# Kernel tuning notes

Hardware: AMD Instinct MI355X
Metric: run time of the kernel (lower is better)

## Reference

```python
import jax, jax.numpy as jnp
import numpy as np

DIM = 1024
H = 16
DH = DIM // H
K = 4
B = 8
N = 2048
EPS = 1e-6


def _depthwise_conv_silu(x, w, n):
    # x: (B, N, C), w: (C, 1, K)  -- torch Conv1d depthwise, padding=K//2, truncate to n, SiLU
    pad = K // 2
    y = jax.lax.conv_general_dilated(
        x.transpose(0, 2, 1), w, window_strides=(1,), padding=[(pad, pad)],
        dimension_numbers=('NCH', 'OIH', 'NCH'), feature_group_count=x.shape[-1])
    y = y[..., :n]  # for even K the conv output is n+1; torch truncates
    return jax.nn.silu(y).transpose(0, 2, 1)


def _l2norm(x):
    return x / (jnp.linalg.norm(x, axis=-1, keepdims=True) + EPS)


def setup_inputs() -> dict:
    key = jax.random.key(0)
    ks = jax.random.split(key, 16)
    s = 1.0 / np.sqrt(DIM)
    d = dict(
        x=jax.random.normal(ks[0], (B, N, DIM), jnp.float32),
        Wq=jax.random.normal(ks[1], (DIM, DIM), jnp.float32) * s,
        bq=jnp.zeros((DIM,), jnp.float32),
        Wk=jax.random.normal(ks[2], (DIM, DIM), jnp.float32) * s,
        bk=jnp.zeros((DIM,), jnp.float32),
        Wv=jax.random.normal(ks[3], (DIM, DIM), jnp.float32) * s,
        bv=jnp.zeros((DIM,), jnp.float32),
        Wa=jax.random.normal(ks[4], (H, DIM), jnp.float32) * s,
        ba=jnp.zeros((H,), jnp.float32),
        Wb=jax.random.normal(ks[5], (H, DIM), jnp.float32) * s,
        bb=jnp.zeros((H,), jnp.float32),
        conv_q=jax.random.normal(ks[6], (DIM, 1, K), jnp.float32) * 0.5,
        conv_k=jax.random.normal(ks[7], (DIM, 1, K), jnp.float32) * 0.5,
        conv_v=jax.random.normal(ks[8], (DIM, 1, K), jnp.float32) * 0.5,
        Wo=jax.random.normal(ks[9], (DIM, DIM), jnp.float32) * s,
        bo=jnp.zeros((DIM,), jnp.float32),
    )
    return d


def _forward(x, Wq, bq, Wk, bk, Wv, bv, Wa, ba, Wb, bb, conv_q, conv_k, conv_v, Wo, bo):
    b_, n_, c_ = x.shape
    q = _l2norm(_depthwise_conv_silu(jax.nn.silu(x @ Wq.T + bq), conv_q, n_))
    k = _l2norm(_depthwise_conv_silu(jax.nn.silu(x @ Wk.T + bk), conv_k, n_))
    v = _depthwise_conv_silu(jax.nn.silu(x @ Wv.T + bv), conv_v, n_)
    a = jax.nn.sigmoid(x @ Wa.T + ba)  # (B, N, H)
    bgate = jax.nn.sigmoid(x @ Wb.T + bb)  # (B, N, H)

    # (N, B, H, Dh) for scan over time
    q = q.reshape(b_, n_, H, DH).transpose(1, 0, 2, 3)
    k = k.reshape(b_, n_, H, DH).transpose(1, 0, 2, 3)
    v = v.reshape(b_, n_, H, DH).transpose(1, 0, 2, 3)
    a = a.transpose(1, 0, 2)
    bgate = bgate.transpose(1, 0, 2)

    S0 = jnp.zeros((b_, H, DH, DH), x.dtype)

    def step(S, inp):
        qt, kt, vt, at, bt = inp  # qt/kt/vt: (B,H,Dh), at/bt: (B,H)
        at = at[..., None, None]
        bt = bt[..., None, None]
        # S_new = S @ (a*(I - b k k^T)) + b * v k^T
        #       = a*S - a*b*(S k) k^T + b * v k^T
        Sk = jnp.einsum('bhde,bhe->bhd', S, kt)
        outer_Sk_k = Sk[..., :, None] * kt[..., None, :]
        outer_v_k = vt[..., :, None] * kt[..., None, :]
        S_new = at * S - at * bt * outer_Sk_k + bt * outer_v_k
        # o_e = sum_d q_d S[d, e]
        ot = jnp.einsum('bhd,bhde->bhe', qt, S_new)
        return S_new, ot

    _, O = jax.lax.scan(step, S0, (q, k, v, a, bgate))  # O: (N, B, H, Dh)
    O = O.transpose(1, 0, 2, 3).reshape(b_, n_, c_)
    return O @ Wo.T + bo


def reference(x, Wq, bq, Wk, bk, Wv, bv, Wa, ba, Wb, bb, conv_q, conv_k, conv_v, Wo, bo):
    return _forward(x, Wq, bq, Wk, bk, Wv, bv, Wa, ba, Wb, bb, conv_q, conv_k, conv_v, Wo, bo)
```

## Files before the change

kernel.cpp:

```cpp
#include <hip/hip_runtime.h>

#define DIMC 1024
#define SEQ  2048
#define NHEAD 16
#define BATCH 8

__device__ __forceinline__ void gll4(const float* g, float* l) {
  __builtin_amdgcn_global_load_lds(
      (const __attribute__((address_space(1))) void*)g,
      (__attribute__((address_space(3))) void*)l, 4, 0, 0);
}
__device__ __forceinline__ void gll16(const unsigned short* g, unsigned short* l) {
  __builtin_amdgcn_global_load_lds(
      (const __attribute__((address_space(1))) void*)g,
      (__attribute__((address_space(3))) void*)l, 16, 0, 0);
}

#define WAIT_VM45   0x8F7D
#define WAIT_VM0    0x0F70

__device__ __forceinline__ unsigned short f2bf(float f) {
  unsigned u = __float_as_uint(f);
  return (unsigned short)((u + 0x7fffu + ((u >> 16) & 1u)) >> 16);
}
__device__ __forceinline__ float bf2f(unsigned short h) {
  return __uint_as_float(((unsigned)h) << 16);
}

typedef __attribute__((ext_vector_type(8))) short  bf16x8;
typedef __attribute__((ext_vector_type(4))) float  floatx4;

__device__ __forceinline__ float oct_sum(float x) {
  int t1 = __builtin_amdgcn_update_dpp(0, __float_as_int(x), 0xB1, 0xF, 0xF, true);
  float x1 = x + __int_as_float(t1);
  int t2 = __builtin_amdgcn_update_dpp(0, __float_as_int(x1), 0x4E, 0xF, 0xF, true);
  float x2 = x1 + __int_as_float(t2);
  int t3 = __builtin_amdgcn_update_dpp(0, __float_as_int(x2), 0x141, 0xF, 0xF, true);
  return x2 + __int_as_float(t3);
}

__global__ __launch_bounds__(256)
void cvt_split(const float* __restrict__ in, unsigned short* __restrict__ hi,
               unsigned short* __restrict__ lo, int n4)
{
  int i = blockIdx.x * 256 + threadIdx.x;
  if (i >= n4) return;
  float4 f = ((const float4*)in)[i];
  unsigned short h0 = f2bf(f.x), h1 = f2bf(f.y), h2 = f2bf(f.z), h3 = f2bf(f.w);
  unsigned short l0 = f2bf(f.x - bf2f(h0)), l1 = f2bf(f.y - bf2f(h1));
  unsigned short l2 = f2bf(f.z - bf2f(h2)), l3 = f2bf(f.w - bf2f(h3));
  ushort4 H; H.x = h0; H.y = h1; H.z = h2; H.w = h3;
  ushort4 L; L.x = l0; L.y = l1; L.z = l2; L.w = l3;
  ((ushort4*)hi)[i] = H;
  ((ushort4*)lo)[i] = L;
}

__global__ void pack_ab_kernel(const float* __restrict__ Wa, const float* __restrict__ ba,
                               const float* __restrict__ Wb, const float* __restrict__ bb,
                               float* __restrict__ Wab, float* __restrict__ bab)
{
  int i = blockIdx.x * 256 + threadIdx.x;
  if (i < 128 * 1024) {
    int row = i >> 10, col = i & 1023;
    float v = 0.0f;
    if (row < 16) v = Wa[(row << 10) + col];
    else if (row < 32) v = Wb[((row - 16) << 10) + col];
    Wab[i] = v;
  } else {
    int j = i - 128 * 1024;
    if (j < 128) {
      float v = 0.0f;
      if (j < 16) v = ba[j];
      else if (j < 32) v = bb[j - 16];
      bab[j] = v;
    }
  }
}

__global__ __launch_bounds__(256, 2)
void gemm_bf16x3(const unsigned short* __restrict__ Ah, const unsigned short* __restrict__ Al,
                 const unsigned short* __restrict__ Bh, const unsigned short* __restrict__ Bl,
                 const float* __restrict__ bias, float* __restrict__ C,
                 int K, int ldc, int nvalid, int act)
{
  __shared__ unsigned short sAh[4096], sAl[4096], sBh[4096], sBl[4096];
  const int tid  = threadIdx.x;
  const int lane = tid & 63;
  const int w    = tid >> 6;

  const int crow = tid >> 2;
  const int kel  = (tid & 3) << 3;
  const unsigned short* pAh0 = Ah + (size_t)(blockIdx.x * 128 + crow) * K + kel;
  const unsigned short* pAh1 = Ah + (size_t)(blockIdx.x * 128 + 64 + crow) * K + kel;
  const unsigned short* pAl0 = Al + (size_t)(blockIdx.x * 128 + crow) * K + kel;
  const unsigned short* pAl1 = Al + (size_t)(blockIdx.x * 128 + 64 + crow) * K + kel;
  const unsigned short* pBh0 = Bh + (size_t)(blockIdx.y * 128 + crow) * K + kel;
  const unsigned short* pBh1 = Bh + (size_t)(blockIdx.y * 128 + 64 + crow) * K + kel;
  const unsigned short* pBl0 = Bl + (size_t)(blockIdx.y * 128 + crow) * K + kel;
  const unsigned short* pBl1 = Bl + (size_t)(blockIdx.y * 128 + 64 + crow) * K + kel;
  const int wb = (tid & 192) * 8;

  floatx4 acc[16];
  #pragma unroll
  for (int i = 0; i < 16; ++i) acc[i] = (floatx4){0.f, 0.f, 0.f, 0.f};

  const int mq = (w & 1) << 6;
  const int nq = (w >> 1) << 6;
  const int fr = lane & 15;
  const int fk = (lane >> 4) << 3;

  for (int kt = 0; kt < K; kt += 32) {
    __syncthreads();
    gll16(pAh0, sAh + wb); gll16(pAh1, sAh + 2048 + wb);
    gll16(pAl0, sAl + wb); gll16(pAl1, sAl + 2048 + wb);
    gll16(pBh0, sBh + wb); gll16(pBh1, sBh + 2048 + wb);
    gll16(pBl0, sBl + wb); gll16(pBl1, sBl + 2048 + wb);
    pAh0 += 32; pAh1 += 32; pAl0 += 32; pAl1 += 32;
    pBh0 += 32; pBh1 += 32; pBl0 += 32; pBl1 += 32;
    __syncthreads();

    bf16x8 ah[4], al[4], bh[4], bl[4];
    #pragma unroll
    for (int mi = 0; mi < 4; ++mi) {
      int off = (mq + mi * 16 + fr) * 32 + fk;
      ah[mi] = *(const bf16x8*)&sAh[off];
      al[mi] = *(const bf16x8*)&sAl[off];
    }
    #pragma unroll
    for (int ni = 0; ni < 4; ++ni) {
      int off = (nq + ni * 16 + fr) * 32 + fk;
      bh[ni] = *(const bf16x8*)&sBh[off];
      bl[ni] = *(const bf16x8*)&sBl[off];
    }
    #pragma unroll
    for (int mi = 0; mi < 4; ++mi)
      #pragma unroll
      for (int ni = 0; ni < 4; ++ni) {
        floatx4 c = acc[mi * 4 + ni];
        c = __builtin_amdgcn_mfma_f32_16x16x32_bf16(ah[mi], bh[ni], c, 0, 0, 0);
        c = __builtin_amdgcn_mfma_f32_16x16x32_bf16(ah[mi], bl[ni], c, 0, 0, 0);
        c = __builtin_amdgcn_mfma_f32_16x16x32_bf16(al[mi], bh[ni], c, 0, 0, 0);
        acc[mi * 4 + ni] = c;
      }
  }

  const int mbase = blockIdx.x * 128 + mq + ((lane >> 4) << 2);
  const int nbase = blockIdx.y * 128 + nq + (lane & 15);
  #pragma unroll
  for (int ni = 0; ni < 4; ++ni) {
    int n = nbase + ni * 16;
    if (n < nvalid) {
      float bs = bias[n];
      #pragma unroll
      for (int mi = 0; mi < 4; ++mi) {
        #pragma unroll
        for (int r = 0; r < 4; ++r) {
          int m = mbase + mi * 16 + r;
          float val = acc[mi * 4 + ni][r] + bs;
          if (act == 1)      val = val * (1.0f / (1.0f + __expf(-val)));
          else if (act == 2) val = 1.0f / (1.0f + __expf(-val));
          C[(size_t)m * ldc + n] = val;
        }
      }
    }
  }
}

__global__ __launch_bounds__(256)
void conv_kernel(const float* __restrict__ pre, const float* __restrict__ w,
                 float* __restrict__ out, int do_norm)
{
  __shared__ float red[4];
  const int bt  = blockIdx.x;
  const int t   = bt & (SEQ - 1);
  const int tid = threadIdx.x;
  const int c   = tid << 2;
  const float* rowp = pre + (size_t)bt * DIMC + c;
  const float4 z = make_float4(0.f, 0.f, 0.f, 0.f);
  float4 xm2 = (t >= 2)      ? *(const float4*)(rowp - 2 * DIMC) : z;
  float4 xm1 = (t >= 1)      ? *(const float4*)(rowp - DIMC)     : z;
  float4 x0  =                 *(const float4*)(rowp);
  float4 xp1 = (t + 1 < SEQ) ? *(const float4*)(rowp + DIMC)     : z;
  const float4 w0 = *(const float4*)(w + (size_t)(c + 0) * 4);
  const float4 w1 = *(const float4*)(w + (size_t)(c + 1) * 4);
  const float4 w2 = *(const float4*)(w + (size_t)(c + 2) * 4);
  const float4 w3 = *(const float4*)(w + (size_t)(c + 3) * 4);
  float y0 = xm2.x * w0.x + xm1.x * w0.y + x0.x * w0.z + xp1.x * w0.w;
  float y1 = xm2.y * w1.x + xm1.y * w1.y + x0.y * w1.z + xp1.y * w1.w;
  float y2 = xm2.z * w2.x + xm1.z * w2.y + x0.z * w2.z + xp1.z * w2.w;
  float y3 = xm2.w * w3.x + xm1.w * w3.y + x0.w * w3.z + xp1.w * w3.w;
  y0 = y0 * (1.0f / (1.0f + __expf(-y0)));
  y1 = y1 * (1.0f / (1.0f + __expf(-y1)));
  y2 = y2 * (1.0f / (1.0f + __expf(-y2)));
  y3 = y3 * (1.0f / (1.0f + __expf(-y3)));
  if (do_norm) {
    float ss = y0*y0 + y1*y1 + y2*y2 + y3*y3;
    #pragma unroll
    for (int off = 32; off >= 1; off >>= 1) ss += __shfl_xor(ss, off);
    if ((tid & 63) == 0) red[tid >> 6] = ss;
    __syncthreads();
    float tot = red[0] + red[1] + red[2] + red[3];
    float rn = 1.0f / (sqrtf(tot) + 1e-6f);
    y0 *= rn; y1 *= rn; y2 *= rn; y3 *= rn;
  }
  *(float4*)(out + (size_t)bt * DIMC + c) = make_float4(y0, y1, y2, y3);
}

#define PD 16
__global__ __launch_bounds__(64)
void scan2_kernel(const float* __restrict__ k, const float* __restrict__ v,
                  const float* __restrict__ ab, float* __restrict__ Cf,
                  float* __restrict__ SC)
{
  __shared__ float ring[PD][2][64];
  __shared__ float aS[SEQ];
  __shared__ float bSh[SEQ];
  const int blk = blockIdx.x;
  const int bh  = blk >> 3;
  const int dg  = blk & 7;
  const int b   = bh >> 4, h = bh & 15;
  const int tid = threadIdx.x;
  const int dl  = tid >> 3;
  const int eh  = tid & 7;
  const int d   = dg * 8 + dl;
  const int e0  = eh * 8;

  const float* abbase = ab + (size_t)b * SEQ * 32 + h;
  for (int i = tid; i < SEQ; i += 64) {
    aS[i]  = abbase[(size_t)i * 32];
    bSh[i] = abbase[(size_t)i * 32 + 16];
  }

  const size_t base = (size_t)b * SEQ * DIMC + h * 64;
  const float* kp = k + base + tid;
  const float* vp = v + base + tid;

  {
    float4 z4 = make_float4(0.f, 0.f, 0.f, 0.f);
    float4* dst0 = (float4*)&SC[(((size_t)bh * 32) * 64 + d) * 64 + e0];
    dst0[0] = z4; dst0[1] = z4;
  }

  #pragma unroll
  for (int pt = 0; pt < PD; ++pt) {
    gll4(kp + (size_t)pt * DIMC, &ring[pt][0][0]);
    gll4(vp + (size_t)pt * DIMC, &ring[pt][1][0]);
  }
  __builtin_amdgcn_s_waitcnt(WAIT_VM0);
  asm volatile("" ::: "memory");

  float S[8];
  #pragma unroll
  for (int j = 0; j < 8; ++j) S[j] = 0.f;

  float* cfp = Cf + (size_t)bh * SEQ * 64 + d;

  float4 ka  = *(const float4*)&ring[0][0][e0];
  float4 kb8 = *(const float4*)&ring[0][0][e0 + 4];
  float  vd  = ring[0][1][d];
  float  a   = aS[0];
  float  bg  = bSh[0];

  for (int t = 0; t < SEQ; ++t) {
    float p0 = fmaf(S[0], ka.x, S[4] * kb8.x);
    float p1 = fmaf(S[1], ka.y, S[5] * kb8.y);
    float p2 = fmaf(S[2], ka.z, S[6] * kb8.z);
    float p3 = fmaf(S[3], ka.w, S[7] * kb8.w);
    float sk = oct_sum((p0 + p1) + (p2 + p3));
    const float coef = fmaf(-a * bg, sk, bg * vd);
    if (eh == 0) cfp[(size_t)t * 64] = coef;
    asm volatile("" ::: "memory");

    if (t < SEQ - PD) {
      const int slot = t & (PD - 1);
      gll4(kp + (size_t)(t + PD) * DIMC, &ring[slot][0][0]);
      gll4(vp + (size_t)(t + PD) * DIMC, &ring[slot][1][0]);
      asm volatile("" ::: "memory");
      __builtin_amdgcn_s_waitcnt(WAIT_VM45);
    } else {
      asm volatile("" ::: "memory");
      __builtin_amdgcn_s_waitcnt(WAIT_VM0);
    }
    asm volatile("" ::: "memory");

    const int sl1 = (t + 1) & (PD - 1);
    const int tn  = (t + 1) & (SEQ - 1);
    const float4 ka_n  = *(const float4*)&ring[sl1][0][e0];
    const float4 kb_n  = *(const float4*)&ring[sl1][0][e0 + 4];
    const float  vd_n  = ring[sl1][1][d];
    const float  a_n   = aS[tn];
    const float  b_n   = bSh[tn];

    S[0] = fmaf(a, S[0], coef * ka.x);
    S[1] = fmaf(a, S[1], coef * ka.y);
    S[2] = fmaf(a, S[2], coef * ka.z);
    S[3] = fmaf(a, S[3], coef * ka.w);
    S[4] = fmaf(a, S[4], coef * kb8.x);
    S[5] = fmaf(a, S[5], coef * kb8.y);
    S[6] = fmaf(a, S[6], coef * kb8.z);
    S[7] = fmaf(a, S[7], coef * kb8.w);

    if (((t + 1) & 63) == 0 && (t + 1) < SEQ) {
      float4* dst = (float4*)&SC[(((size_t)bh * 32 + ((t + 1) >> 6)) * 64 + d) * 64 + e0];
      dst[0] = make_float4(S[0], S[1], S[2], S[3]);
      dst[1] = make_float4(S[4], S[5], S[6], S[7]);
    }

    ka = ka_n; kb8 = kb_n; vd = vd_n; a = a_n; bg = b_n;
  }
}

__global__ __launch_bounds__(256)
void outp_kernel(const float* __restrict__ q, const float* __restrict__ k,
                 const float* __restrict__ Cf, const float* __restrict__ SC,
                 const float* __restrict__ ab, float* __restrict__ O)
{
  __shared__ float QsT[64 * 64];
  __shared__ float CP [64 * 64];
  __shared__ float Ks [64 * 64];
  __shared__ float Zs [64 * 64];
  __shared__ float av[64], Gv[64], rGv[64];

  const int c   = blockIdx.x;
  const int bh  = blockIdx.y;
  const int b   = bh >> 4, h = bh & 15;
  const int cs  = c << 6;
  const int tid = threadIdx.x;
  const int tl  = tid & 63, th = tid >> 6;

  {
    const float* qr = q  + ((size_t)(b * SEQ + cs + tl)) * DIMC + h * 64 + th * 16;
    const float* cr = Cf + ((size_t)bh * SEQ + cs + tl) * 64 + th * 16;
    #pragma unroll
    for (int u = 0; u < 4; ++u) {
      float4 qv = *(const float4*)(qr + u * 4);
      float4 cv = *(const float4*)(cr + u * 4);
      int dd = th * 16 + u * 4;
      QsT[(dd+0)*64 + tl] = qv.x; QsT[(dd+1)*64 + tl] = qv.y;
      QsT[(dd+2)*64 + tl] = qv.z; QsT[(dd+3)*64 + tl] = qv.w;
      CP [(dd+0)*64 + tl] = cv.x; CP [(dd+1)*64 + tl] = cv.y;
      CP [(dd+2)*64 + tl] = cv.z; CP [(dd+3)*64 + tl] = cv.w;
    }
    const float* kr = k  + ((size_t)(b * SEQ + cs + tl)) * DIMC + h * 64 + th * 16;
    const float* zr = SC + (((size_t)bh * 32 + c) * 64 + tl) * 64 + th * 16;
    #pragma unroll
    for (int u = 0; u < 4; ++u) {
      *(float4*)&Ks[tl * 64 + th * 16 + u * 4] = *(const float4*)(kr + u * 4);
      *(float4*)&Zs[tl * 64 + th * 16 + u * 4] = *(const float4*)(zr + u * 4);
    }
    if (tid < 64) av[tid] = ab[((size_t)(b * SEQ + cs + tid)) * 32 + h];
  }
  __syncthreads();
  if (tid == 0) {
    float g = 1.f;
    for (int t = 0; t < 64; ++t) { g *= av[t]; Gv[t] = fmaxf(g, 1e-37f); }
  }
  __syncthreads();
  if (tid < 64) rGv[tid] = 1.0f / Gv[tid];
  __syncthreads();

  const int tq = (tid >> 4) << 2;
  const int s0 = (tid & 15) << 2;

  float p[4][4] = {{0.f}};
  #pragma unroll 4
  for (int dd = 0; dd < 64; ++dd) {
    const float4 qv = *(const float4*)&QsT[dd * 64 + tq];
    const float4 cv = *(const float4*)&CP [dd * 64 + s0];
    const float qa[4] = {qv.x, qv.y, qv.z, qv.w};
    const float ca[4] = {cv.x, cv.y, cv.z, cv.w};
    #pragma unroll
    for (int i = 0; i < 4; ++i)
      #pragma unroll
      for (int j = 0; j < 4; ++j)
        p[i][j] = fmaf(qa[i], ca[j], p[i][j]);
  }
  __syncthreads();

  #pragma unroll
  for (int i = 0; i < 4; ++i) {
    const float gt = Gv[tq + i];
    #pragma unroll
    for (int j = 0; j < 4; ++j) {
      float vsc = (s0 + j <= tq + i) ? p[i][j] * gt * rGv[s0 + j] : 0.f;
      CP[(s0 + j) * 64 + (tq + i)] = vsc;
    }
  }
  __syncthreads();

  const int e0 = s0;
  float o[4][4] = {{0.f}};
  #pragma unroll 4
  for (int ss = 0; ss < 64; ++ss) {
    const float4 pv = *(const float4*)&CP[ss * 64 + tq];
    const float4 kv = *(const float4*)&Ks[ss * 64 + e0];
    const float pa[4] = {pv.x, pv.y, pv.z, pv.w};
    const float ka[4] = {kv.x, kv.y, kv.z, kv.w};
    #pragma unroll
    for (int i = 0; i < 4; ++i)
      #pragma unroll
      for (int j = 0; j < 4; ++j)
        o[i][j] = fmaf(pa[i], ka[j], o[i][j]);
  }
  float zt[4][4] = {{0.f}};
  #pragma unroll 4
  for (int dd = 0; dd < 64; ++dd) {
    const float4 qv = *(const float4*)&QsT[dd * 64 + tq];
    const float4 zv = *(const float4*)&Zs[dd * 64 + e0];
    const float qa[4] = {qv.x, qv.y, qv.z, qv.w};
    const float za[4] = {zv.x, zv.y, zv.z, zv.w};
    #pragma unroll
    for (int i = 0; i < 4; ++i)
      #pragma unroll
      for (int j = 0; j < 4; ++j)
        zt[i][j] = fmaf(qa[i], za[j], zt[i][j]);
  }
  #pragma unroll
  for (int i = 0; i < 4; ++i) {
    const float gt = Gv[tq + i];
    float4 res;
    res.x = fmaf(gt, zt[i][0], o[i][0]);
    res.y = fmaf(gt, zt[i][1], o[i][1]);
    res.z = fmaf(gt, zt[i][2], o[i][2]);
    res.w = fmaf(gt, zt[i][3], o[i][3]);
    *(float4*)(O + ((size_t)(b * SEQ + cs + tq + i)) * DIMC + h * 64 + e0) = res;
  }
}

extern "C" void kernel_launch(void* const* d_in, const int* in_sizes, int n_in,
                              void* d_out, int out_size, void* d_ws, size_t ws_size,
                              hipStream_t stream)
{
  const float* x  = (const float*)d_in[0];
  const float* Wq = (const float*)d_in[1];
  const float* bq = (const float*)d_in[2];
  const float* Wk = (const float*)d_in[3];
  const float* bk = (const float*)d_in[4];
  const float* Wv = (const float*)d_in[5];
  const float* bv = (const float*)d_in[6];
  const float* Wa = (const float*)d_in[7];
  const float* ba = (const float*)d_in[8];
  const float* Wb = (const float*)d_in[9];
  const float* bb = (const float*)d_in[10];
  const float* cq = (const float*)d_in[11];
  const float* ck = (const float*)d_in[12];
  const float* cv = (const float*)d_in[13];
  const float* Wo = (const float*)d_in[14];
  const float* bo = (const float*)d_in[15];
  float* out = (float*)d_out;
  float* ws  = (float*)d_ws;

  const size_t per_b = (size_t)SEQ * DIMC;
  const size_t wsz   = (size_t)DIMC * DIMC;

  int bc = BATCH;
  while (bc > 1) {
    size_t fl = 4 * (size_t)bc * per_b + (size_t)bc * SEQ * 32 + 128 * 1024 + 128;
    size_t us = 2 * (size_t)bc * per_b + 8 * wsz + 2 * 128 * 1024;
    if (fl * 4 + us * 2 <= ws_size) break;
    bc >>= 1;
  }

  float* P   = ws;
  float* qb  = P  + (size_t)bc * per_b;
  float* kb  = qb + (size_t)bc * per_b;
  float* vb  = kb + (size_t)bc * per_b;
  float* abb = vb + (size_t)bc * per_b;
  float* Wab = abb + (size_t)bc * SEQ * 32;
  float* bab = Wab + 128 * 1024;
  unsigned short* xh   = (unsigned short*)(bab + 128);
  unsigned short* xl   = xh  + (size_t)bc * per_b;
  unsigned short* wqh  = xl  + (size_t)bc * per_b;
  unsigned short* wql  = wqh + wsz;
  unsigned short* wkh  = wql + wsz;
  unsigned short* wkl  = wkh + wsz;
  unsigned short* wvh  = wkl + wsz;
  unsigned short* wvl  = wvh + wsz;
  unsigned short* woh  = wvl + wsz;
  unsigned short* wol  = woh + wsz;
  unsigned short* wabh = wol + wsz;
  unsigned short* wabl = wabh + 128 * 1024;

  float* Cf  = (float*)xh;
  float* SCp = P;

  pack_ab_kernel<<<513, 256, 0, stream>>>(Wa, ba, Wb, bb, Wab, bab);
  cvt_split<<<(int)(wsz / 4 + 255) / 256, 256, 0, stream>>>(Wq, wqh, wql, (int)(wsz / 4));
  cvt_split<<<(int)(wsz / 4 + 255) / 256, 256, 0, stream>>>(Wk, wkh, wkl, (int)(wsz / 4));
  cvt_split<<<(int)(wsz / 4 + 255) / 256, 256, 0, stream>>>(Wv, wvh, wvl, (int)(wsz / 4));
  cvt_split<<<(int)(wsz / 4 + 255) / 256, 256, 0, stream>>>(Wo, woh, wol, (int)(wsz / 4));
  cvt_split<<<(128 * 1024 / 4 + 255) / 256, 256, 0, stream>>>(Wab, wabh, wabl, 128 * 1024 / 4);

  for (int b0 = 0; b0 < BATCH; b0 += bc) {
    const float* xb = x + (size_t)b0 * per_b;
    const int M = bc * SEQ;
    const int n4 = (int)((size_t)bc * per_b / 4);
    dim3 gg(M / 128, DIMC / 128);
    dim3 gab(M / 128, 1);

    cvt_split<<<(n4 + 255) / 256, 256, 0, stream>>>(xb, xh, xl, n4);

    gemm_bf16x3<<<gg, 256, 0, stream>>>(xh, xl, wqh, wql, bq, P, DIMC, DIMC, DIMC, 1);
    conv_kernel<<<dim3(M), 256, 0, stream>>>(P, cq, qb, 1);
    gemm_bf16x3<<<gg, 256, 0, stream>>>(xh, xl, wkh, wkl, bk, P, DIMC, DIMC, DIMC, 1);
    conv_kernel<<<dim3(M), 256, 0, stream>>>(P, ck, kb, 1);
    gemm_bf16x3<<<gg, 256, 0, stream>>>(xh, xl, wvh, wvl, bv, P, DIMC, DIMC, DIMC, 1);
    conv_kernel<<<dim3(M), 256, 0, stream>>>(P, cv, vb, 0);
    gemm_bf16x3<<<gab, 256, 0, stream>>>(xh, xl, wabh, wabl, bab, abb, DIMC, 32, 32, 2);
    scan2_kernel<<<dim3(bc * NHEAD * 8), 64, 0, stream>>>(kb, vb, abb, Cf, SCp);
    outp_kernel<<<dim3(SEQ / 64, bc * NHEAD), 256, 0, stream>>>(qb, kb, Cf, SCp, abb, vb);
    cvt_split<<<(n4 + 255) / 256, 256, 0, stream>>>(vb, xh, xl, n4);
    gemm_bf16x3<<<gg, 256, 0, stream>>>(xh, xl, woh, wol, bo, out + (size_t)b0 * per_b, DIMC, DIMC, DIMC, 0);
  }
}
```

Measured before the change: 1.808 ms.

## Unroll recurrent state scan by two timesteps with algebraic fusion of updates

The sequential delta-rule scan now processes two timesteps per iteration. It computes S·k for both keys and the k1·k2 inner product from the same old state, derives the second coefficient algebraically, and applies a single combined rank-2 state update. This roughly halves the serial dependency chain of cross-lane reductions and state updates per timestep. The cost is extra FMAs and a third reduction per pair, slightly different rounding, and a retuned waitcnt for the doubled prefetch loads.

Result: faster. 1.620 ms (-10.4%).

```diff
diff --git a/kernel.cpp b/kernel.cpp
--- a/kernel.cpp
+++ b/kernel.cpp
@@ -16,7 +16,7 @@
       (__attribute__((address_space(3))) void*)l, 16, 0, 0);
 }
 
-#define WAIT_VM45   0x8F7D
+#define WAIT_VM42   0x8F7A
 #define WAIT_VM0    0x0F70
 
 __device__ __forceinline__ unsigned short f2bf(float f) {
@@ -220,9 +220,8 @@
   const int dg  = blk & 7;
   const int b   = bh >> 4, h = bh & 15;
   const int tid = threadIdx.x;
-  const int dl  = tid >> 3;
   const int eh  = tid & 7;
-  const int d   = dg * 8 + dl;
+  const int d   = dg * 8 + (tid >> 3);
   const int e0  = eh * 8;
 
   const float* abbase = ab + (size_t)b * SEQ * 32 + h;
@@ -255,58 +254,86 @@
 
   float* cfp = Cf + (size_t)bh * SEQ * 64 + d;
 
-  float4 ka  = *(const float4*)&ring[0][0][e0];
-  float4 kb8 = *(const float4*)&ring[0][0][e0 + 4];
-  float  vd  = ring[0][1][d];
-  float  a   = aS[0];
-  float  bg  = bSh[0];
-
-  for (int t = 0; t < SEQ; ++t) {
-    float p0 = fmaf(S[0], ka.x, S[4] * kb8.x);
-    float p1 = fmaf(S[1], ka.y, S[5] * kb8.y);
-    float p2 = fmaf(S[2], ka.z, S[6] * kb8.z);
-    float p3 = fmaf(S[3], ka.w, S[7] * kb8.w);
-    float sk = oct_sum((p0 + p1) + (p2 + p3));
-    const float coef = fmaf(-a * bg, sk, bg * vd);
-    if (eh == 0) cfp[(size_t)t * 64] = coef;
+  float4 k1a = *(const float4*)&ring[0][0][e0];
+  float4 k1b = *(const float4*)&ring[0][0][e0 + 4];
+  float4 k2a = *(const float4*)&ring[1][0][e0];
+  float4 k2b = *(const float4*)&ring[1][0][e0 + 4];
+  float  v1  = ring[0][1][d];
+  float  v2  = ring[1][1][d];
+  float  a1  = aS[0], a2 = aS[1];
+  float  b1  = bSh[0], b2 = bSh[1];
+
+  for (int t = 0; t < SEQ; t += 2) {
+    float q0 = fmaf(S[0], k1a.x, S[4] * k1b.x);
+    float q1 = fmaf(S[1], k1a.y, S[5] * k1b.y);
+    float q2 = fmaf(S[2], k1a.z, S[6] * k1b.z);
+    float q3 = fmaf(S[3], k1a.w, S[7] * k1b.w);
+    float r0 = fmaf(S[0], k2a.x, S[4] * k2b.x);
+    float r1 = fmaf(S[1], k2a.y, S[5] * k2b.y);
+    float r2 = fmaf(S[2], k2a.z, S[6] * k2b.z);
+    float r3 = fmaf(S[3], k2a.w, S[7] * k2b.w);
+    float x0 = fmaf(k1a.x, k2a.x, k1b.x * k2b.x);
+    float x1 = fmaf(k1a.y, k2a.y, k1b.y * k2b.y);
+    float x2 = fmaf(k1a.z, k2a.z, k1b.z * k2b.z);
+    float x3 = fmaf(k1a.w, k2a.w, k1b.w * k2b.w);
+    float u1  = oct_sum((q0 + q1) + (q2 + q3));
+    float u2  = oct_sum((r0 + r1) + (r2 + r3));
+    float kap = oct_sum((x0 + x1) + (x2 + x3));
+
+    const float e1 = b1 * v1, f1 = a1 * b1;
+    const float e2 = b2 * v2, f2 = a2 * b2;
+    const float w2 = a1 * u2;
+    const float G2 = a1 * a2;
+    const float c1 = fmaf(-f1, u1, e1);
+    const float c2 = fmaf(-f2, fmaf(c1, kap, w2), e2);
+    const float d1 = a2 * c1;
+    if (eh == 0) { cfp[(size_t)t * 64] = c1; cfp[(size_t)(t + 1) * 64] = c2; }
     asm volatile("" ::: "memory");
 
     if (t < SEQ - PD) {
-      const int slot = t & (PD - 1);
-      gll4(kp + (size_t)(t + PD) * DIMC, &ring[slot][0][0]);
-      gll4(vp + (size_t)(t + PD) * DIMC, &ring[slot][1][0]);
+      const int s0 = t & (PD - 1);
+      const int s1 = (t + 1) & (PD - 1);
+      gll4(kp + (size_t)(t + PD) * DIMC,     &ring[s0][0][0]);
+      gll4(vp + (size_t)(t + PD) * DIMC,     &ring[s0][1][0]);
+      gll4(kp + (size_t)(t + PD + 1) * DIMC, &ring[s1][0][0]);
+      gll4(vp + (size_t)(t + PD + 1) * DIMC, &ring[s1][1][0]);
       asm volatile("" ::: "memory");
-      __builtin_amdgcn_s_waitcnt(WAIT_VM45);
+      __builtin_amdgcn_s_waitcnt(WAIT_VM42);
     } else {
       asm volatile("" ::: "memory");
       __builtin_amdgcn_s_waitcnt(WAIT_VM0);
     }
     asm volatile("" ::: "memory");
 
-    const int sl1 = (t + 1) & (PD - 1);
-    const int tn  = (t + 1) & (SEQ - 1);
-    const float4 ka_n  = *(const float4*)&ring[sl1][0][e0];
-    const float4 kb_n  = *(const float4*)&ring[sl1][0][e0 + 4];
-    const float  vd_n  = ring[sl1][1][d];
-    const float  a_n   = aS[tn];
-    const float  b_n   = bSh[tn];
-
-    S[0] = fmaf(a, S[0], coef * ka.x);
-    S[1] = fmaf(a, S[1], coef * ka.y);
-    S[2] = fmaf(a, S[2], coef * ka.z);
-    S[3] = fmaf(a, S[3], coef * ka.w);
-    S[4] = fmaf(a, S[4], coef * kb8.x);
-    S[5] = fmaf(a, S[5], coef * kb8.y);
-    S[6] = fmaf(a, S[6], coef * kb8.z);
-    S[7] = fmaf(a, S[7], coef * kb8.w);
-
-    if (((t + 1) & 63) == 0 && (t + 1) < SEQ) {
-      float4* dst = (float4*)&SC[(((size_t)bh * 32 + ((t + 1) >> 6)) * 64 + d) * 64 + e0];
+    const int sl2 = (t + 2) & (PD - 1);
+    const int sl3 = (t + 3) & (PD - 1);
+    const int tn  = (t + 2) & (SEQ - 1);
+    const float4 k1a_n = *(const float4*)&ring[sl2][0][e0];
+    const float4 k1b_n = *(const float4*)&ring[sl2][0][e0 + 4];
+    const float4 k2a_n = *(const float4*)&ring[sl3][0][e0];
+    const float4 k2b_n = *(const float4*)&ring[sl3][0][e0 + 4];
+    const float  v1_n  = ring[sl2][1][d];
+    const float  v2_n  = ring[sl3][1][d];
+    const float2 a_n   = *(const float2*)&aS[tn];
+    const float2 b_n   = *(const float2*)&bSh[tn];
+
+    S[0] = fmaf(G2, S[0], fmaf(d1, k1a.x, c2 * k2a.x));
+    S[1] = fmaf(G2, S[1], fmaf(d1, k1a.y, c2 * k2a.y));
+    S[2] = fmaf(G2, S[2], fmaf(d1, k1a.z, c2 * k2a.z));
+    S[3] = fmaf(G2, S[3], fmaf(d1, k1a.w, c2 * k2a.w));
+    S[4] = fmaf(G2, S[4], fmaf(d1, k1b.x, c2 * k2b.x));
+    S[5] = fmaf(G2, S[5], fmaf(d1, k1b.y, c2 * k2b.y));
+    S[6] = fmaf(G2, S[6], fmaf(d1, k1b.z, c2 * k2b.z));
+    S[7] = fmaf(G2, S[7], fmaf(d1, k1b.w, c2 * k2b.w));
+
+    if (((t + 2) & 63) == 0 && (t + 2) < SEQ) {
+      float4* dst = (float4*)&SC[(((size_t)bh * 32 + ((t + 2) >> 6)) * 64 + d) * 64 + e0];
       dst[0] = make_float4(S[0], S[1], S[2], S[3]);
       dst[1] = make_float4(S[4], S[5], S[6], S[7]);
     }
 
-    ka = ka_n; kb8 = kb_n; vd = vd_n; a = a_n; bg = b_n;
+    k1a = k1a_n; k1b = k1b_n; k2a = k2a_n; k2b = k2b_n;
+    v1 = v1_n; v2 = v2_n; a1 = a_n.x; a2 = a_n.y; b1 = b_n.x; b2 = b_n.y;
   }
 }
 
```
